# Optimization experiments

Hardware: AMD Instinct MI355X
Metric: run time of the kernel (lower is better)

Reference implementation:

```python
import jax, jax.numpy as jnp
import numpy as np
import math

J = 4096          # input_output_size
B = 4096          # batch
S = 4             # n_samples
PI = 0.5          # mixture weight
SIGMA1 = 1.0
SIGMA2 = 0.002
RHO_SCALE = -5.0
MU_SCALE = math.sqrt(6.0 / J)
LOG_SQRT_2PI = 0.5 * math.log(2.0 * math.pi)


def _normal_logpdf(x, mu, sigma):
    # elementwise Normal log-density
    return -LOG_SQRT_2PI - jnp.log(sigma) - (x - mu) ** 2 / (2.0 * sigma ** 2)


def setup_inputs() -> dict:
    key = jax.random.key(0)
    k1, k2, k3 = jax.random.split(key, 3)
    x = jax.random.normal(k1, (B, J), dtype=jnp.float32)
    weight_mu = jax.random.uniform(k2, (J,), dtype=jnp.float32,
                                   minval=-MU_SCALE, maxval=MU_SCALE)
    weight_rho = jnp.full((J,), RHO_SCALE, dtype=jnp.float32)
    eps = jax.random.normal(k3, (S, J), dtype=jnp.float32)
    return {"x": x, "weight_mu": weight_mu, "weight_rho": weight_rho,
            "eps": eps, "n_samples": S}


def reference(x, weight_mu, weight_rho, eps, n_samples):
    # reparameterized weight sample: [S, J]
    sigma = jnp.log1p(jnp.exp(weight_rho))            # softplus, [J]
    weight = weight_mu + sigma * eps                  # [S, J]

    # variational posterior log-prob: sum over samples and features
    log_variational_posterior = jnp.sum(_normal_logpdf(weight, weight_mu, sigma))

    # scale-mixture Gaussian prior log-prob (stable via logaddexp)
    lp1 = _normal_logpdf(weight, 0.0, jnp.float32(SIGMA1)) + jnp.log(jnp.float32(PI))
    lp2 = _normal_logpdf(weight, 0.0, jnp.float32(SIGMA2)) + jnp.log(jnp.float32(1.0 - PI))
    log_prior = jnp.sum(jnp.logaddexp(lp1, lp2))

    # einsum('bj,jk->bjk', w, eye) then einsum('bij,bjk->bik', x, .)
    # is mathematically out[s,b,j] = x[b,j] * weight[s,j]
    out = x[None, :, :] * weight[:, None, :]          # [S, B, J]
    return out, log_prior, log_variational_posterior
```

## Files before the change

### kernel.cpp

```cpp
#include <hip/hip_runtime.h>
#include <math.h>

#define LOG_SQRT_2PI 0.9189385332046727f

typedef float f32x4 __attribute__((ext_vector_type(4)));

__device__ __forceinline__
void reduce_duty(const float* __restrict__ mu,
                 const float* __restrict__ rho,
                 const float* __restrict__ eps,
                 float* __restrict__ out_scalars,
                 double* __restrict__ ws,
                 int S, int J, int nRed)
{
    const int n = S * J;
    double lvp = 0.0, lpr = 0.0;
    const float log_half   = -0.6931471805599453f;
    const float log_sigma2 = -6.214608098422191f;
    const float inv_2s2_2  = 125000.0f;

    for (int idx = blockIdx.x * blockDim.x + threadIdx.x; idx < n;
         idx += nRed * blockDim.x) {
        const int j = idx % J;
        const float m = mu[j];
        const float r = rho[j];
        const float e = eps[idx];
        const float sg = log1pf(expf(r));
        const float w  = m + sg * e;

        const float d = w - m;
        lvp += (double)(-LOG_SQRT_2PI - logf(sg) - (d * d) / (2.0f * sg * sg));

        const float w2  = w * w;
        const float lp1 = -LOG_SQRT_2PI - 0.5f * w2 + log_half;
        const float lp2 = -LOG_SQRT_2PI - log_sigma2 - w2 * inv_2s2_2 + log_half;
        const float mx  = fmaxf(lp1, lp2);
        const float mn  = fminf(lp1, lp2);
        lpr += (double)(mx + log1pf(expf(mn - mx)));
    }

    for (int off = 32; off > 0; off >>= 1) {
        lvp += __shfl_down(lvp, off, 64);
        lpr += __shfl_down(lpr, off, 64);
    }
    __shared__ double s_l[2][4];
    const int wid = threadIdx.x >> 6, lane = threadIdx.x & 63;
    if (lane == 0) { s_l[0][wid] = lvp; s_l[1][wid] = lpr; }
    __syncthreads();
    if (threadIdx.x == 0) {
        const int nw = blockDim.x >> 6;
        double bl_lvp = 0.0, bl_lpr = 0.0;
        for (int i = 0; i < nw; ++i) { bl_lvp += s_l[0][i]; bl_lpr += s_l[1][i]; }
        atomicAdd(&ws[0], bl_lpr);
        atomicAdd(&ws[1], bl_lvp);
        __threadfence();
        unsigned int* counter = (unsigned int*)(ws + 2);
        const unsigned int prev = atomicAdd(counter, 1u);
        if (prev == (unsigned)(nRed - 1)) {
            __threadfence();
            out_scalars[0] = (float)atomicAdd(&ws[0], 0.0);
            out_scalars[1] = (float)atomicAdd(&ws[1], 0.0);
        }
    }
}

__global__ __launch_bounds__(256)
void bel_fused4(const f32x4* __restrict__ x4,
                const float* __restrict__ mu,
                const float* __restrict__ rho,
                const float* __restrict__ eps,
                f32x4* __restrict__ o4,
                float* __restrict__ out_scalars,
                double* __restrict__ ws,
                int B, int J, int jblocks, int nRed)
{
    if ((int)blockIdx.x < nRed)
        reduce_duty(mu, rho, eps, out_scalars, ws, 4, J, nRed);

    const int Jv      = J >> 2;
    const int jb      = blockIdx.x % jblocks;
    const int bstart  = blockIdx.x / jblocks;
    const int bstride = gridDim.x / jblocks;
    const int jv      = jb * blockDim.x + threadIdx.x;
    if (jv >= Jv) return;

    const f32x4 muv  = ((const f32x4*)mu)[jv];
    const f32x4 rhov = ((const f32x4*)rho)[jv];
    f32x4 sg;
    sg.x = log1pf(expf(rhov.x));
    sg.y = log1pf(expf(rhov.y));
    sg.z = log1pf(expf(rhov.z));
    sg.w = log1pf(expf(rhov.w));

    const f32x4 e0 = ((const f32x4*)eps)[0 * Jv + jv];
    const f32x4 e1 = ((const f32x4*)eps)[1 * Jv + jv];
    const f32x4 e2 = ((const f32x4*)eps)[2 * Jv + jv];
    const f32x4 e3 = ((const f32x4*)eps)[3 * Jv + jv];

    const f32x4 w0 = muv + sg * e0;
    const f32x4 w1 = muv + sg * e1;
    const f32x4 w2 = muv + sg * e2;
    const f32x4 w3 = muv + sg * e3;

    const size_t plane = (size_t)B * Jv;

    #pragma unroll 4
    for (int b = bstart; b < B; b += bstride) {
        const size_t rb = (size_t)b * Jv + jv;
        const f32x4 xv = x4[rb];
        __builtin_nontemporal_store(xv * w0, &o4[0 * plane + rb]);
        __builtin_nontemporal_store(xv * w1, &o4[1 * plane + rb]);
        __builtin_nontemporal_store(xv * w2, &o4[2 * plane + rb]);
        __builtin_nontemporal_store(xv * w3, &o4[3 * plane + rb]);
    }
}

__global__ __launch_bounds__(256)
void bel_reduce_gen(const float* __restrict__ mu, const float* __restrict__ rho,
                    const float* __restrict__ eps, float* __restrict__ out_scalars,
                    double* __restrict__ ws, int S, int J, int nRed)
{
    reduce_duty(mu, rho, eps, out_scalars, ws, S, J, nRed);
}

__global__ __launch_bounds__(256)
void bel_scale_gen(const f32x4* __restrict__ x4,
                   const float* __restrict__ mu, const float* __restrict__ rho,
                   const float* __restrict__ eps, f32x4* __restrict__ o4,
                   long long total4, int Jv, int B, int S)
{
    long long idx = (long long)blockIdx.x * blockDim.x + threadIdx.x;
    const long long stride = (long long)gridDim.x * blockDim.x;
    const long long plane = (long long)B * Jv;
    for (; idx < (long long)S * plane; idx += stride) {
        const int s  = (int)(idx / plane);
        const long long r = idx % plane;
        const int jv = (int)(r % Jv);
        const f32x4 muv  = ((const f32x4*)mu)[jv];
        const f32x4 rhov = ((const f32x4*)rho)[jv];
        const f32x4 ev   = ((const f32x4*)eps)[(long long)s * Jv + jv];
        const f32x4 xv   = x4[r];
        f32x4 sg;
        sg.x = log1pf(expf(rhov.x));
        sg.y = log1pf(expf(rhov.y));
        sg.z = log1pf(expf(rhov.z));
        sg.w = log1pf(expf(rhov.w));
        const f32x4 ov = xv * (muv + sg * ev);
        __builtin_nontemporal_store(ov, &o4[idx]);
    }
}

extern "C" void kernel_launch(void* const* d_in, const int* in_sizes, int n_in,
                              void* d_out, int out_size, void* d_ws, size_t ws_size,
                              hipStream_t stream) {
    const float* x   = (const float*)d_in[0];
    const float* mu  = (const float*)d_in[1];
    const float* rho = (const float*)d_in[2];
    const float* eps = (const float*)d_in[3];

    const int J = in_sizes[1];
    const int B = in_sizes[0] / J;
    const int S = in_sizes[3] / J;

    float* out = (float*)d_out;
    float* out_scalars = out + (size_t)S * B * J;
    double* ws = (double*)d_ws;

    (void)hipMemsetAsync(d_ws, 0, 24, stream);

    const int nRed = 32;
    const int block = 256;
    const int Jv = J / 4;

    if (S == 4 && (Jv % block) == 0) {
        const int jblocks  = Jv / block;
        const int bstride  = (B < 1024) ? B : 1024;
        const int grid     = jblocks * bstride;
        bel_fused4<<<grid, block, 0, stream>>>(
            (const f32x4*)x, mu, rho, eps, (f32x4*)out, out_scalars, ws,
            B, J, jblocks, nRed);
    } else {
        bel_reduce_gen<<<nRed, block, 0, stream>>>(mu, rho, eps, out_scalars, ws, S, J, nRed);
        const long long total4 = (long long)S * B * Jv;
        long long blocks = (total4 + block - 1) / block;
        if (blocks > 2048) blocks = 2048;
        bel_scale_gen<<<(int)blocks, block, 0, stream>>>(
            (const f32x4*)x, mu, rho, eps, (f32x4*)out, total4, Jv, B, S);
    }
}
```

Baseline: 336.5 us.

## Process two column chunks per thread and use regular stores instead of nontemporal

Each thread in the fused kernel now covers two float4 column chunks, which halves the number of j-blocks and the grid, and interleaves eight output stores per batch row. Nontemporal stores are replaced with ordinary stores in both the fused and generic paths, changing how the 256 MB output write interacts with the cache. The aim is more memory-level parallelism per thread and possibly better write coalescing. The cost is more registers per thread and half as many blocks, so each thread does twice as much work.

```diff
diff --git a/kernel.cpp b/kernel.cpp
--- a/kernel.cpp
+++ b/kernel.cpp
@@ -72,46 +72,52 @@
                 f32x4* __restrict__ o4,
                 float* __restrict__ out_scalars,
                 double* __restrict__ ws,
-                int B, int J, int jblocks, int nRed)
+                int B, int J, int jblocks, int bstride, int nRed)
 {
     if ((int)blockIdx.x < nRed)
         reduce_duty(mu, rho, eps, out_scalars, ws, 4, J, nRed);
 
-    const int Jv      = J >> 2;
-    const int jb      = blockIdx.x % jblocks;
-    const int bstart  = blockIdx.x / jblocks;
-    const int bstride = gridDim.x / jblocks;
-    const int jv      = jb * blockDim.x + threadIdx.x;
-    if (jv >= Jv) return;
+    const int Jv  = J >> 2;
+    const int TW  = blockDim.x * 2;
+    const int jb  = blockIdx.x % jblocks;
+    const int bstart = blockIdx.x / jblocks;
+    const int jv0 = jb * TW + threadIdx.x;
+    const int jv1 = jv0 + blockDim.x;
 
-    const f32x4 muv  = ((const f32x4*)mu)[jv];
-    const f32x4 rhov = ((const f32x4*)rho)[jv];
-    f32x4 sg;
-    sg.x = log1pf(expf(rhov.x));
-    sg.y = log1pf(expf(rhov.y));
-    sg.z = log1pf(expf(rhov.z));
-    sg.w = log1pf(expf(rhov.w));
+    const f32x4* muv  = (const f32x4*)mu;
+    const f32x4* rhov = (const f32x4*)rho;
+    const f32x4* ev   = (const f32x4*)eps;
 
-    const f32x4 e0 = ((const f32x4*)eps)[0 * Jv + jv];
-    const f32x4 e1 = ((const f32x4*)eps)[1 * Jv + jv];
-    const f32x4 e2 = ((const f32x4*)eps)[2 * Jv + jv];
-    const f32x4 e3 = ((const f32x4*)eps)[3 * Jv + jv];
-
-    const f32x4 w0 = muv + sg * e0;
-    const f32x4 w1 = muv + sg * e1;
-    const f32x4 w2 = muv + sg * e2;
-    const f32x4 w3 = muv + sg * e3;
+    f32x4 w[2][4];
+    #pragma unroll
+    for (int c = 0; c < 2; ++c) {
+        const int jv = c ? jv1 : jv0;
+        const f32x4 m = muv[jv];
+        const f32x4 r = rhov[jv];
+        f32x4 sg;
+        sg.x = log1pf(expf(r.x)); sg.y = log1pf(expf(r.y));
+        sg.z = log1pf(expf(r.z)); sg.w = log1pf(expf(r.w));
+        #pragma unroll
+        for (int s = 0; s < 4; ++s)
+            w[c][s] = m + sg * ev[s * Jv + jv];
+    }
 
     const size_t plane = (size_t)B * Jv;
 
     #pragma unroll 4
     for (int b = bstart; b < B; b += bstride) {
-        const size_t rb = (size_t)b * Jv + jv;
-        const f32x4 xv = x4[rb];
-        __builtin_nontemporal_store(xv * w0, &o4[0 * plane + rb]);
-        __builtin_nontemporal_store(xv * w1, &o4[1 * plane + rb]);
-        __builtin_nontemporal_store(xv * w2, &o4[2 * plane + rb]);
-        __builtin_nontemporal_store(xv * w3, &o4[3 * plane + rb]);
+        const size_t r0 = (size_t)b * Jv + jv0;
+        const size_t r1 = (size_t)b * Jv + jv1;
+        const f32x4 x0 = x4[r0];
+        const f32x4 x1 = x4[r1];
+        o4[0 * plane + r0] = x0 * w[0][0];
+        o4[0 * plane + r1] = x1 * w[1][0];
+        o4[1 * plane + r0] = x0 * w[0][1];
+        o4[1 * plane + r1] = x1 * w[1][1];
+        o4[2 * plane + r0] = x0 * w[0][2];
+        o4[2 * plane + r1] = x1 * w[1][2];
+        o4[3 * plane + r0] = x0 * w[0][3];
+        o4[3 * plane + r1] = x1 * w[1][3];
     }
 }
 
@@ -138,15 +144,12 @@
         const int jv = (int)(r % Jv);
         const f32x4 muv  = ((const f32x4*)mu)[jv];
         const f32x4 rhov = ((const f32x4*)rho)[jv];
-        const f32x4 ev   = ((const f32x4*)eps)[(long long)s * Jv + jv];
+        const f32x4 evv  = ((const f32x4*)eps)[(long long)s * Jv + jv];
         const f32x4 xv   = x4[r];
         f32x4 sg;
-        sg.x = log1pf(expf(rhov.x));
-        sg.y = log1pf(expf(rhov.y));
-        sg.z = log1pf(expf(rhov.z));
-        sg.w = log1pf(expf(rhov.w));
-        const f32x4 ov = xv * (muv + sg * ev);
-        __builtin_nontemporal_store(ov, &o4[idx]);
+        sg.x = log1pf(expf(rhov.x)); sg.y = log1pf(expf(rhov.y));
+        sg.z = log1pf(expf(rhov.z)); sg.w = log1pf(expf(rhov.w));
+        o4[idx] = xv * (muv + sg * evv);
     }
 }
 
@@ -171,14 +174,16 @@
     const int nRed = 32;
     const int block = 256;
     const int Jv = J / 4;
+    const int TW = block * 2;
 
-    if (S == 4 && (Jv % block) == 0) {
-        const int jblocks  = Jv / block;
-        const int bstride  = (B < 1024) ? B : 1024;
-        const int grid     = jblocks * bstride;
+    if (S == 4 && (Jv % TW) == 0 && B >= 4) {
+        const int jblocks = Jv / TW;
+        int bstride = 1024;
+        if (bstride > B) bstride = B;
+        const int grid = jblocks * bstride;
         bel_fused4<<<grid, block, 0, stream>>>(
             (const f32x4*)x, mu, rho, eps, (f32x4*)out, out_scalars, ws,
-            B, J, jblocks, nRed);
+            B, J, jblocks, bstride, nRed);
     } else {
         bel_reduce_gen<<<nRed, block, 0, stream>>>(mu, rho, eps, out_scalars, ws, S, J, nRed);
         const long long total4 = (long long)S * B * Jv;
```

After: 334.7 us. Within noise of the previous version (-0.5%).
